# Optimization experiments

Hardware: AMD Instinct MI355X
Metric: run time of the kernel (lower is better)

Reference implementation:

```python
import jax, jax.numpy as jnp
import numpy as np

DIM = 512      # model dim
HEADS = 8
DH = DIM // HEADS          # 64, dim_head
M = DIM // 2               # 256, num_landmarks
ITERS = 6                  # pinv_iterations
K = 33                     # residual_conv_kernel (lucidrains default)
B, N = 4, 4096             # N divisible by M -> no padding branch


def setup_inputs() -> dict:
    key = jax.random.key(0)
    ks = jax.random.split(key, 5)
    s = 0.02
    return {
        "x": jax.random.normal(ks[0], (B, N, DIM), jnp.float32),
        "ln_w": jnp.ones((DIM,), jnp.float32),
        "ln_b": jnp.zeros((DIM,), jnp.float32),
        "w_qkv": jax.random.normal(ks[1], (DIM, 3 * HEADS * DH), jnp.float32) * s,
        "w_out": jax.random.normal(ks[2], (HEADS * DH, DIM), jnp.float32) * s,
        "b_out": jnp.zeros((DIM,), jnp.float32),
        "w_conv": jax.random.normal(ks[3], (HEADS, 1, K, 1), jnp.float32) * s,  # depthwise Conv2d (h,1,33,1)
    }


def _moore_penrose_pinv(x, iters=ITERS):
    # Newton-Schulz iterative pseudo-inverse, as in lucidrains nystrom-attention
    abs_x = jnp.abs(x)
    col = abs_x.sum(-1)
    row = abs_x.sum(-2)
    z = jnp.swapaxes(x, -1, -2) / (jnp.max(col) * jnp.max(row))  # global max, matching torch.max
    I = jnp.eye(x.shape[-1], dtype=x.dtype)
    for _ in range(iters):
        xz = x @ z
        z = 0.25 * z @ (13.0 * I - xz @ (15.0 * I - xz @ (7.0 * I - xz)))
    return z


def reference(x, ln_w, ln_b, w_qkv, w_out, b_out, w_conv):
    b, n, d = x.shape
    # LayerNorm (biased variance, eps=1e-5 as torch default)
    mu = jnp.mean(x, -1, keepdims=True)
    var = jnp.mean(jnp.square(x - mu), -1, keepdims=True)
    xn = (x - mu) / jnp.sqrt(var + 1e-5) * ln_w + ln_b

    qkv = xn @ w_qkv                                   # [b,n,3*h*dh]
    q, k, v = jnp.split(qkv, 3, axis=-1)
    split = lambda t: t.reshape(b, n, HEADS, DH).transpose(0, 2, 1, 3)  # [b,h,n,dh]
    q, k, v = split(q), split(k), split(v)
    q = q * (DH ** -0.5)

    l = n // M                                         # tokens per landmark
    q_l = q.reshape(b, HEADS, M, l, DH).mean(axis=3)   # [b,h,m,dh]
    k_l = k.reshape(b, HEADS, M, l, DH).mean(axis=3)

    sim1 = jnp.einsum('bhid,bhjd->bhij', q, k_l)       # [b,h,n,m]
    sim2 = jnp.einsum('bhid,bhjd->bhij', q_l, k_l)     # [b,h,m,m]
    sim3 = jnp.einsum('bhid,bhjd->bhij', q_l, k)       # [b,h,m,n]
    a1 = jax.nn.softmax(sim1, -1)
    a2 = jax.nn.softmax(sim2, -1)
    a3 = jax.nn.softmax(sim3, -1)

    a2_inv = _moore_penrose_pinv(a2)
    out = (a1 @ a2_inv) @ (a3 @ v)                     # [b,h,n,dh]

    # depthwise residual conv over sequence dim (kernel (33,1), groups=heads)
    res = jax.lax.conv_general_dilated(
        v, w_conv, window_strides=(1, 1),
        padding=((K // 2, K // 2), (0, 0)),
        dimension_numbers=('NCHW', 'OIHW', 'NCHW'),
        feature_group_count=HEADS)
    out = out + res

    out = out.transpose(0, 2, 1, 3).reshape(b, n, HEADS * DH)
    out = out @ w_out + b_out
    return x + out
```

## Files before the change

kernel.cpp:

```cpp
#include <hip/hip_runtime.h>
#include <cstdint>

typedef __bf16 bf16;
typedef __bf16 bf16x8 __attribute__((ext_vector_type(8)));
typedef float  f32x4  __attribute__((ext_vector_type(4)));

__device__ __forceinline__ void glds16(const void* g, void* l) {
  __builtin_amdgcn_global_load_lds((const __attribute__((address_space(1))) void*)g,
                                   (__attribute__((address_space(3))) void*)l, 16, 0, 0);
}

__global__ __launch_bounds__(256) void prep_w(const float* __restrict__ wqkv, const float* __restrict__ wout,
                                              bf16* __restrict__ wqkvT, bf16* __restrict__ woutT) {
  int idx = blockIdx.x * 256 + threadIdx.x;
  if (idx < 98304) {
    int r8 = idx & 63, c = idx >> 6;
    bf16 o[8];
#pragma unroll
    for (int e = 0; e < 8; e++) o[e] = (bf16)wqkv[(long)(r8 * 8 + e) * 1536 + c];
    *(uint4*)(wqkvT + (long)c * 512 + r8 * 8) = *(uint4*)o;
  } else {
    int j = idx - 98304;
    int r8 = j & 63, c = j >> 6;
    bf16 o[8];
#pragma unroll
    for (int e = 0; e < 8; e++) o[e] = (bf16)wout[(long)(r8 * 8 + e) * 512 + c];
    *(uint4*)(woutT + (long)c * 512 + r8 * 8) = *(uint4*)o;
  }
}

__global__ __launch_bounds__(64) void ln_kernel(const float* __restrict__ x,
    const float* __restrict__ w, const float* __restrict__ b, bf16* __restrict__ xn) {
  long row = blockIdx.x;
  int t = threadIdx.x;
  const float* rp = x + row * 512 + t * 8;
  float4 p0 = *(const float4*)rp;
  float4 p1 = *(const float4*)(rp + 4);
  float vals[8] = {p0.x, p0.y, p0.z, p0.w, p1.x, p1.y, p1.z, p1.w};
  float s = 0.f, s2 = 0.f;
#pragma unroll
  for (int e = 0; e < 8; e++) { s += vals[e]; s2 += vals[e] * vals[e]; }
#pragma unroll
  for (int o = 32; o > 0; o >>= 1) { s += __shfl_xor(s, o); s2 += __shfl_xor(s2, o); }
  float mu = s * (1.f / 512.f);
  float var = s2 * (1.f / 512.f) - mu * mu;
  float rstd = rsqrtf(var + 1e-5f);
  float4 w0 = *(const float4*)(w + t * 8), w1 = *(const float4*)(w + t * 8 + 4);
  float4 b0 = *(const float4*)(b + t * 8), b1 = *(const float4*)(b + t * 8 + 4);
  float wv[8] = {w0.x, w0.y, w0.z, w0.w, w1.x, w1.y, w1.z, w1.w};
  float bv[8] = {b0.x, b0.y, b0.z, b0.w, b1.x, b1.y, b1.z, b1.w};
  bf16 outv[8];
#pragma unroll
  for (int e = 0; e < 8; e++) outv[e] = (bf16)((vals[e] - mu) * rstd * wv[e] + bv[e]);
  *(uint4*)(xn + row * 512 + t * 8) = *(uint4*)outv;
}

enum { MODE_BF16 = 1, MODE_QKV = 2, MODE_RESID = 3, MODE_XZ = 4, MODE_DIAG = 5, MODE_Y0 = 6, MODE_ZY = 7 };

template <int KDIM, int MODE>
__global__ __launch_bounds__(256) void gemm_ns(
    const bf16* __restrict__ A, const bf16* __restrict__ B, void* __restrict__ C,
    int N, long sA, long sB, long sC, float alpha, float cdiag,
    const float* __restrict__ scal, bf16* __restrict__ aux0, bf16* __restrict__ aux1) {
  constexpr int BM = 64;
  __shared__ __align__(16) bf16 As[BM * KDIM];
  __shared__ __align__(16) bf16 Bs[BM * KDIM];
  const int tid = threadIdx.x, lane = tid & 63, wave = tid >> 6;
  const int quad = lane >> 4, l16 = lane & 15;
  constexpr int LPR = KDIM / 8;
  constexpr int CPW = (BM * KDIM / 512) / 4;
  constexpr int RPC = 64 / LPR;
  const int bm0 = blockIdx.x * BM, bn0 = blockIdx.y * BM;
  const bf16* Ab = A + (long)blockIdx.z * sA;
  const bf16* Bb = B + (long)(MODE == MODE_ZY ? (blockIdx.z & 31) : blockIdx.z) * sB;

  const int rin = lane / LPR, gr = lane % LPR;
#pragma unroll
  for (int t = 0; t < CPW; t++) {
    int seg = wave * CPW + t;
    int row = seg * RPC + rin;
    int scol = 8 * (gr ^ (row & 7));
    glds16(&Ab[(long)(bm0 + row) * KDIM + scol], &As[seg * 512]);
    glds16(&Bb[(long)(bn0 + row) * KDIM + scol], &Bs[seg * 512]);
  }
  __syncthreads();

  f32x4 zero = {0.f, 0.f, 0.f, 0.f};
  f32x4 acc[4];
#pragma unroll
  for (int j = 0; j < 4; j++) acc[j] = zero;
  const int arow = wave * 16 + l16;
  const int aswz = (l16 & 7) * 8;
#pragma unroll
  for (int ki = 0; ki < KDIM / 32; ki++) {
    int cph = (ki * 32 + quad * 8) ^ aswz;
    bf16x8 af = *(const bf16x8*)&As[arow * KDIM + cph];
    bf16x8 bfr[4];
#pragma unroll
    for (int j = 0; j < 4; j++)
      bfr[j] = *(const bf16x8*)&Bs[(j * 16 + l16) * KDIM + cph];
#pragma unroll
    for (int j = 0; j < 4; j++)
      acc[j] = __builtin_amdgcn_mfma_f32_16x16x32_bf16(af, bfr[j], acc[j], 0, 0, 0);
  }

  const long cb = (long)blockIdx.z * sC;
  float rscale = 1.f;
  if (MODE == MODE_Y0) rscale = 1.f / (scal[0] * scal[1]);
#pragma unroll
  for (int j = 0; j < 4; j++)
#pragma unroll
    for (int r = 0; r < 4; r++) {
      int row = bm0 + wave * 16 + quad * 4 + r;
      int col = bn0 + j * 16 + l16;
      float v = acc[j][r] * alpha;
      if (MODE == MODE_BF16) {
        ((bf16*)C)[cb + (long)row * N + col] = (bf16)v;
      } else if (MODE == MODE_Y0) {
        long o = cb + (long)row * N + col;
        float vv = v * rscale;
        aux0[o] = (bf16)vv;
        aux1[o] = (bf16)(((row == col) ? cdiag : 0.f) - vv);
      } else if (MODE == MODE_ZY) {
        long o = cb + (long)row * N + col;
        ((bf16*)C)[o] = (bf16)v;
        if (blockIdx.z >= 32) aux1[o - 2097152] = (bf16)(((row == col) ? cdiag : 0.f) - v);
      } else if (MODE == MODE_DIAG) {
        ((bf16*)C)[cb + (long)row * N + col] = (bf16)(((row == col) ? cdiag : 0.f) - v);
      }
    }
}

template <int BM, int MODE>
__global__ __launch_bounds__(256) void gemm_g(
    const bf16* __restrict__ A, const bf16* __restrict__ B, void* __restrict__ C,
    int N, int K, long sA, long sB, long sC, float alpha, float cdiag,
    const float* __restrict__ resid, const float* __restrict__ bias,
    bf16* __restrict__ aux0, bf16* __restrict__ aux1, bf16* __restrict__ aux2) {
  constexpr int BK = 32, BN = BM;
  __shared__ __align__(16) bf16 As[BM * BK];
  __shared__ __align__(16) bf16 Bs[BN * BK];
  const int tid = threadIdx.x, lane = tid & 63, wave = tid >> 6;
  const int quad = lane >> 4, l16 = lane & 15;
  constexpr int WN = (BN >= 128) ? 2 : 1;
  constexpr int WM = 4 / WN;
  constexpr int TM = BM / (WM * 16), TN = BN / (WN * 16);
  constexpr int ISS = BM / 64;
  const int wm0 = (wave / WN) * (BM / WM);
  const int wn0 = (wave % WN) * (BN / WN);
  const int bm0 = blockIdx.x * BM, bn0 = blockIdx.y * BN;
  const bf16* Ab = A + (long)blockIdx.z * sA;
  const bf16* Bb = B + (long)blockIdx.z * sB;
  const int srow = lane >> 2, scol = (lane & 3) * 8;

  f32x4 zero = {0.f, 0.f, 0.f, 0.f};
  f32x4 acc[TM][TN];
#pragma unroll
  for (int i = 0; i < TM; i++)
#pragma unroll
    for (int j = 0; j < TN; j++) acc[i][j] = zero;

  for (int k0 = 0; k0 < K; k0 += BK) {
#pragma unroll
    for (int t = 0; t < ISS; t++) {
      int seg = wave * ISS + t;
      glds16(&Ab[(long)(bm0 + seg * 16 + srow) * K + k0 + scol], &As[seg * 512]);
      glds16(&Bb[(long)(bn0 + seg * 16 + srow) * K + k0 + scol], &Bs[seg * 512]);
    }
    __syncthreads();
    bf16x8 af[TM], bfr[TN];
#pragma unroll
    for (int i = 0; i < TM; i++)
      af[i] = *(const bf16x8*)&As[(wm0 + i * 16 + l16) * BK + quad * 8];
#pragma unroll
    for (int j = 0; j < TN; j++)
      bfr[j] = *(const bf16x8*)&Bs[(wn0 + j * 16 + l16) * BK + quad * 8];
#pragma unroll
    for (int i = 0; i < TM; i++)
#pragma unroll
      for (int j = 0; j < TN; j++)
        acc[i][j] = __builtin_amdgcn_mfma_f32_16x16x32_bf16(af[i], bfr[j], acc[i][j], 0, 0, 0);
    __syncthreads();
  }

  const long cb = (long)blockIdx.z * sC;
#pragma unroll
  for (int i = 0; i < TM; i++)
#pragma unroll
    for (int j = 0; j < TN; j++)
#pragma unroll
      for (int r = 0; r < 4; r++) {
        int row = bm0 + wm0 + i * 16 + quad * 4 + r;
        int col = bn0 + wn0 + j * 16 + l16;
        float v = acc[i][j][r] * alpha;
        if (MODE == MODE_QKV) {
          int b = row >> 12, n = row & 4095;
          int which = col >> 9, h = (col >> 6) & 7, d = col & 63;
          long o = ((long)(b * 8 + h) * 4096 + n) * 64 + d;
          if (which == 0) aux0[o] = (bf16)(v * 0.125f);
          else if (which == 1) aux1[o] = (bf16)v;
          else aux2[o] = (bf16)v;
        } else {
          long o = (long)row * N + col;
          ((float*)C)[o] = v + bias[col] + resid[o];
        }
      }
}

template <int BM, int BN, bool BT, int MODE>
__global__ __launch_bounds__(256) void gemm_k(
    const bf16* __restrict__ A, const bf16* __restrict__ B, void* __restrict__ C,
    int M, int N, int K, long sA, long sB, long sC, float alpha, float cdiag,
    const float* __restrict__ resid, const float* __restrict__ bias,
    bf16* __restrict__ aux0, bf16* __restrict__ aux1, bf16* __restrict__ aux2) {
  constexpr int BK = 32, LDST = 40;
  __shared__ __align__(16) bf16 As[BM * LDST];
  __shared__ __align__(16) bf16 Bs[BN * LDST];
  const int tid = threadIdx.x, lane = tid & 63, wave = tid >> 6;
  const int quad = lane >> 4, l16 = lane & 15;
  constexpr int WN = (BN >= 128) ? 2 : 1;
  constexpr int WM = 4 / WN;
  constexpr int TM = BM / (WM * 16), TN = BN / (WN * 16);
  const int wm0 = (wave / WN) * (BM / WM);
  const int wn0 = (wave % WN) * (BN / WN);
  const int bm0 = blockIdx.x * BM, bn0 = blockIdx.y * BN;
  const bf16* Ab = A + (long)blockIdx.z * sA;
  const bf16* Bb = B + (long)blockIdx.z * sB;

  f32x4 zero = {0.f, 0.f, 0.f, 0.f};
  f32x4 acc[TM][TN];
#pragma unroll
  for (int i = 0; i < TM; i++)
#pragma unroll
    for (int j = 0; j < TN; j++) acc[i][j] = zero;

  for (int k0 = 0; k0 < K; k0 += BK) {
    for (int c = tid; c < BM * 4; c += 256) {
      int r = c >> 2, cv = (c & 3) * 8;
      *(uint4*)&As[r * LDST + cv] = *(const uint4*)&Ab[(long)(bm0 + r) * K + k0 + cv];
    }
    if (BT) {
      for (int c = tid; c < BN * 4; c += 256) {
        int r = c >> 2, cv = (c & 3) * 8;
        *(uint4*)&Bs[r * LDST + cv] = *(const uint4*)&Bb[(long)(bn0 + r) * K + k0 + cv];
      }
    } else {
      for (int c = tid; c < BN * 4; c += 256) {
        int kk = c / (BN / 8), nv = (c % (BN / 8)) * 8;
        uint4 tmp = *(const uint4*)&Bb[(long)(k0 + kk) * N + bn0 + nv];
        const bf16* tv = (const bf16*)&tmp;
#pragma unroll
        for (int e = 0; e < 8; e++) Bs[(nv + e) * LDST + kk] = tv[e];
      }
    }
    __syncthreads();
    bf16x8 af[TM], bfr[TN];
#pragma unroll
    for (int i = 0; i < TM; i++)
      af[i] = *(const bf16x8*)&As[(wm0 + i * 16 + l16) * LDST + quad * 8];
#pragma unroll
    for (int j = 0; j < TN; j++)
      bfr[j] = *(const bf16x8*)&Bs[(wn0 + j * 16 + l16) * LDST + quad * 8];
#pragma unroll
    for (int i = 0; i < TM; i++)
#pragma unroll
      for (int j = 0; j < TN; j++)
        acc[i][j] = __builtin_amdgcn_mfma_f32_16x16x32_bf16(af[i], bfr[j], acc[i][j], 0, 0, 0);
    __syncthreads();
  }

  const long cb = (long)blockIdx.z * sC;
#pragma unroll
  for (int i = 0; i < TM; i++)
#pragma unroll
    for (int j = 0; j < TN; j++)
#pragma unroll
      for (int r = 0; r < 4; r++) {
        int row = bm0 + wm0 + i * 16 + quad * 4 + r;
        int col = bn0 + wn0 + j * 16 + l16;
        float v = acc[i][j][r] * alpha;
        if (MODE == MODE_BF16) {
          ((bf16*)C)[cb + (long)row * N + col] = (bf16)v;
        }
      }
}

__global__ __launch_bounds__(256) void lm_kernel(const bf16* __restrict__ q, const bf16* __restrict__ k,
                                                 bf16* __restrict__ ql, bf16* __restrict__ kl) {
  int bh = blockIdx.x, mi = blockIdx.y * 4 + (threadIdx.x >> 6), d = threadIdx.x & 63;
  long base = ((long)bh * 4096 + mi * 16) * 64 + d;
  float sq = 0.f, sk = 0.f;
#pragma unroll
  for (int j = 0; j < 16; j++) { sq += (float)q[base + j * 64]; sk += (float)k[base + j * 64]; }
  long o = ((long)bh * 256 + mi) * 64 + d;
  ql[o] = (bf16)(sq * (1.f / 16.f));
  kl[o] = (bf16)(sk * (1.f / 16.f));
}

__global__ __launch_bounds__(256) void softmax256(bf16* __restrict__ buf) {
  long row = blockIdx.x;
  int t = threadIdx.x, lane = t & 63, wave = t >> 6;
  __shared__ float sm[4];
  float v = (float)buf[row * 256 + t];
  float m = v;
#pragma unroll
  for (int o = 32; o > 0; o >>= 1) m = fmaxf(m, __shfl_xor(m, o));
  if (lane == 0) sm[wave] = m;
  __syncthreads();
  m = fmaxf(fmaxf(sm[0], sm[1]), fmaxf(sm[2], sm[3]));
  float e = __expf(v - m);
  __syncthreads();
  float s = e;
#pragma unroll
  for (int o = 32; o > 0; o >>= 1) s += __shfl_xor(s, o);
  if (lane == 0) sm[wave] = s;
  __syncthreads();
  s = sm[0] + sm[1] + sm[2] + sm[3];
  buf[row * 256 + t] = (bf16)(e / s);
}

__global__ void init_scal(float* scal) { scal[0] = 1.0f; ((int*)scal)[1] = 0; }

__global__ __launch_bounds__(64) void red_col(const bf16* __restrict__ a2h, float* scal) {
  int bh = blockIdx.x;
  int j = blockIdx.y * 64 + threadIdx.x;
  float s = 0.f;
  const bf16* p = a2h + (long)bh * 65536 + j;
  for (int i = 0; i < 256; i++) s += (float)p[i * 256];
  atomicMax((int*)scal + 1, __float_as_int(s));
}

__global__ __launch_bounds__(256) void z0_k(const bf16* __restrict__ a2h,
                                            const float* __restrict__ scal, bf16* __restrict__ z) {
  int bh = blockIdx.x, i = blockIdx.y, j = threadIdx.x;
  float inv = 1.f / (scal[0] * scal[1]);
  float v = (float)a2h[((long)bh * 256 + i) * 256 + j];
  z[((long)bh * 256 + j) * 256 + i] = (bf16)(v * inv);
}

__global__ __launch_bounds__(256) void wt_k(const bf16* __restrict__ W, bf16* __restrict__ WT) {
  int bh = blockIdx.x, tid = threadIdx.x;
  const bf16* wb = W + (long)bh * 16384;
  bf16* wtb = WT + (long)bh * 16384;
  for (int i = tid; i < 2048; i += 256) {
    int n = i >> 3, d8 = (i & 7) * 8;
    uint4 pk = *(const uint4*)&wb[n * 64 + d8];
    const bf16* pv = (const bf16*)&pk;
#pragma unroll
    for (int e = 0; e < 8; e++) wtb[(d8 + e) * 256 + n] = pv[e];
  }
}

__global__ __launch_bounds__(256) void f3_partial(const bf16* __restrict__ ql,
    const bf16* __restrict__ k, const bf16* __restrict__ v,
    float* __restrict__ Opart, float* __restrict__ lpart) {
  const int mt = blockIdx.x, ns = blockIdx.y, bh = blockIdx.z;
  const int tid = threadIdx.x, lane = tid & 63, wave = tid >> 6;
  const int quad = lane >> 4, l16 = lane & 15;
  const int wr0 = mt * 128 + wave * 32;
  __shared__ __align__(16) bf16 vT[64][72];
  __shared__ __align__(16) bf16 Pts[4][32][72];

  const bf16* qlb = ql + (long)bh * 16384;
  const bf16* kb  = k + (long)bh * 262144;
  const bf16* vb  = v + (long)bh * 262144;

  bf16x8 aq[2][2];
#pragma unroll
  for (int ti = 0; ti < 2; ti++)
#pragma unroll
    for (int ki = 0; ki < 2; ki++)
      aq[ti][ki] = *(const bf16x8*)&qlb[(wr0 + ti * 16 + l16) * 64 + ki * 32 + quad * 8];

  f32x4 zero = {0.f, 0.f, 0.f, 0.f};
  f32x4 Oacc[2][4];
#pragma unroll
  for (int i = 0; i < 2; i++)
#pragma unroll
    for (int j = 0; j < 4; j++) Oacc[i][j] = zero;
  float lacc[2][4] = {};

  for (int c = 0; c < 8; c++) {
    int n0c = ns * 512 + c * 64;
    __syncthreads();
    for (int i = tid; i < 512; i += 256) {
      int nn = i >> 3, d8 = (i & 7) * 8;
      uint4 pk = *(const uint4*)&vb[(long)(n0c + nn) * 64 + d8];
      const bf16* pv = (const bf16*)&pk;
#pragma unroll
      for (int e = 0; e < 8; e++) vT[d8 + e][nn] = pv[e];
    }
    __syncthreads();

    f32x4 sacc[2][4];
#pragma unroll
    for (int i = 0; i < 2; i++)
#pragma unroll
      for (int j = 0; j < 4; j++) sacc[i][j] = zero;
#pragma unroll
    for (int ki = 0; ki < 2; ki++) {
      bf16x8 bk[4];
#pragma unroll
      for (int tj = 0; tj < 4; tj++)
        bk[tj] = *(const bf16x8*)&kb[(long)(n0c + tj * 16 + l16) * 64 + ki * 32 + quad * 8];
#pragma unroll
      for (int ti = 0; ti < 2; ti++)
#pragma unroll
        for (int tj = 0; tj < 4; tj++)
          sacc[ti][tj] = __builtin_amdgcn_mfma_f32_16x16x32_bf16(aq[ti][ki], bk[tj], sacc[ti][tj], 0, 0, 0);
    }
#pragma unroll
    for (int ti = 0; ti < 2; ti++)
#pragma unroll
      for (int tj = 0; tj < 4; tj++)
#pragma unroll
        for (int r = 0; r < 4; r++) {
          float e = __expf(sacc[ti][tj][r]);
          lacc[ti][r] += e;
          Pts[wave][ti * 16 + quad * 4 + r][tj * 16 + l16] = (bf16)e;
        }
#pragma unroll
    for (int ki = 0; ki < 2; ki++) {
      bf16x8 ap[2], bv[4];
#pragma unroll
      for (int ti = 0; ti < 2; ti++)
        ap[ti] = *(const bf16x8*)&Pts[wave][ti * 16 + l16][ki * 32 + quad * 8];
#pragma unroll
      for (int tj = 0; tj < 4; tj++)
        bv[tj] = *(const bf16x8*)&vT[tj * 16 + l16][ki * 32 + quad * 8];
#pragma unroll
      for (int ti = 0; ti < 2; ti++)
#pragma unroll
        for (int tj = 0; tj < 4; tj++)
          Oacc[ti][tj] = __builtin_amdgcn_mfma_f32_16x16x32_bf16(ap[ti], bv[tj], Oacc[ti][tj], 0, 0, 0);
    }
  }

#pragma unroll
  for (int ti = 0; ti < 2; ti++)
#pragma unroll
    for (int r = 0; r < 4; r++) {
#pragma unroll
      for (int o = 1; o < 16; o <<= 1) lacc[ti][r] += __shfl_xor(lacc[ti][r], o);
    }
  long pb = ((long)bh * 8 + ns) * 256;
#pragma unroll
  for (int ti = 0; ti < 2; ti++)
#pragma unroll
    for (int r = 0; r < 4; r++) {
      int row = wr0 + ti * 16 + quad * 4 + r;
      if (l16 == 0) lpart[pb + row] = lacc[ti][r];
#pragma unroll
      for (int tj = 0; tj < 4; tj++)
        Opart[(pb + row) * 64 + tj * 16 + l16] = Oacc[ti][tj][r];
    }
}

__global__ __launch_bounds__(256) void f3_combine(const float* __restrict__ Opart,
    const float* __restrict__ lpart, bf16* __restrict__ a3v) {
  int row = blockIdx.x * 4 + (threadIdx.x >> 6);
  int d = threadIdx.x & 63;
  int bh = row >> 8, m = row & 255;
  float so = 0.f, sl = 0.f;
#pragma unroll
  for (int s = 0; s < 8; s++) {
    long pb = ((long)bh * 8 + s) * 256 + m;
    so += Opart[pb * 64 + d];
    sl += lpart[pb];
  }
  a3v[(long)row * 64 + d] = (bf16)(so / sl);
}

__global__ __launch_bounds__(256) void f1_attn(const bf16* __restrict__ q,
    const bf16* __restrict__ kl, const bf16* __restrict__ WT, const bf16* __restrict__ v,
    const float* __restrict__ wconv, bf16* __restrict__ xattn) {
  const int nt = blockIdx.x, bh = blockIdx.y;
  const int h = bh & 7, b = bh >> 3, n0 = nt * 64;
  const int tid = threadIdx.x, lane = tid & 63, wave = tid >> 6;
  const int quad = lane >> 4, l16 = lane & 15;
  __shared__ __align__(16) bf16 PtsBuf[64 * 264];
  __shared__ float red[4][64];
  __shared__ float linv[64];
  bf16 (*Pts)[264] = (bf16(*)[264])PtsBuf;
  bf16 (*vsT)[104] = (bf16(*)[104])PtsBuf;

  const bf16* qb  = q + (long)bh * 262144;
  const bf16* klb = kl + (long)bh * 16384;
  const bf16* wtb = WT + (long)bh * 16384;
  const bf16* vb  = v + (long)bh * 262144;

  float wreg = (lane < 33) ? wconv[h * 33 + lane] : 0.f;

  uint4 vstage[3];
#pragma unroll
  for (int t = 0; t < 3; t++) {
    int i = tid + t * 256;
    int r = i >> 3, d8 = (i & 7) * 8;
    int n = n0 - 16 + r;
    uint4 val = {0u, 0u, 0u, 0u};
    if (n >= 0 && n < 4096) val = *(const uint4*)&vb[(long)n * 64 + d8];
    vstage[t] = val;
  }

  f32x4 zero = {0.f, 0.f, 0.f, 0.f};
  f32x4 sacc[4][4];
#pragma unroll
  for (int i = 0; i < 4; i++)
#pragma unroll
    for (int j = 0; j < 4; j++) sacc[i][j] = zero;
#pragma unroll
  for (int ki = 0; ki < 2; ki++) {
    bf16x8 aq[4], bk[4];
#pragma unroll
    for (int ti = 0; ti < 4; ti++)
      aq[ti] = *(const bf16x8*)&qb[(long)(n0 + ti * 16 + l16) * 64 + ki * 32 + quad * 8];
#pragma unroll
    for (int tj = 0; tj < 4; tj++)
      bk[tj] = *(const bf16x8*)&klb[(long)(wave * 64 + tj * 16 + l16) * 64 + ki * 32 + quad * 8];
#pragma unroll
    for (int ti = 0; ti < 4; ti++)
#pragma unroll
      for (int tj = 0; tj < 4; tj++)
        sacc[ti][tj] = __builtin_amdgcn_mfma_f32_16x16x32_bf16(aq[ti], bk[tj], sacc[ti][tj], 0, 0, 0);
  }
  float ps[4][4] = {};
#pragma unroll
  for (int ti = 0; ti < 4; ti++)
#pragma unroll
    for (int tj = 0; tj < 4; tj++)
#pragma unroll
      for (int r = 0; r < 4; r++) {
        float e = __expf(sacc[ti][tj][r]);
        ps[ti][r] += e;
        Pts[ti * 16 + quad * 4 + r][wave * 64 + tj * 16 + l16] = (bf16)e;
      }
#pragma unroll
  for (int ti = 0; ti < 4; ti++)
#pragma unroll
    for (int r = 0; r < 4; r++) {
#pragma unroll
      for (int o = 1; o < 16; o <<= 1) ps[ti][r] += __shfl_xor(ps[ti][r], o);
      if (l16 == 0) red[wave][ti * 16 + quad * 4 + r] = ps[ti][r];
    }
  __syncthreads();
  if (tid < 64) linv[tid] = 1.f / (red[0][tid] + red[1][tid] + red[2][tid] + red[3][tid]);
  __syncthreads();

  const int r0 = wave * 16;
  f32x4 Oacc[4];
#pragma unroll
  for (int j = 0; j < 4; j++) Oacc[j] = zero;
#pragma unroll
  for (int ki = 0; ki < 8; ki++) {
    bf16x8 ap = *(const bf16x8*)&Pts[r0 + l16][ki * 32 + quad * 8];
    bf16x8 bw[4];
#pragma unroll
    for (int tj = 0; tj < 4; tj++)
      bw[tj] = *(const bf16x8*)&wtb[(long)(tj * 16 + l16) * 256 + ki * 32 + quad * 8];
#pragma unroll
    for (int tj = 0; tj < 4; tj++)
      Oacc[tj] = __builtin_amdgcn_mfma_f32_16x16x32_bf16(ap, bw[tj], Oacc[tj], 0, 0, 0);
  }
  __syncthreads();

#pragma unroll
  for (int t = 0; t < 3; t++) {
    int i = tid + t * 256;
    int r = i >> 3, d8 = (i & 7) * 8;
    const bf16* pv = (const bf16*)&vstage[t];
#pragma unroll
    for (int e = 0; e < 8; e++) vsT[d8 + e][r] = pv[e];
  }
  __syncthreads();

  f32x4 Cacc[4];
#pragma unroll
  for (int j = 0; j < 4; j++) Cacc[j] = zero;
#pragma unroll
  for (int ki = 0; ki < 3; ki++) {
    if (ki * 32 + 31 < r0 || ki * 32 > r0 + 47) continue;
    bf16x8 av;
#pragma unroll
    for (int j = 0; j < 8; j++) {
      int idx = ki * 32 + quad * 8 + j - r0 - l16;
      float wv = __shfl(wreg, idx & 63);
      av[j] = (idx >= 0 && idx < 33) ? (bf16)wv : (bf16)0.f;
    }
    bf16x8 bv[4];
#pragma unroll
    for (int tj = 0; tj < 4; tj++)
      bv[tj] = *(const bf16x8*)&vsT[tj * 16 + l16][ki * 32 + quad * 8];
#pragma unroll
    for (int tj = 0; tj < 4; tj++)
      Cacc[tj] = __builtin_amdgcn_mfma_f32_16x16x32_bf16(av, bv[tj], Cacc[tj], 0, 0, 0);
  }

#pragma unroll
  for (int rr = 0; rr < 4; rr++) {
    int row = r0 + quad * 4 + rr;
    float inv = linv[row];
    int n = n0 + row;
#pragma unroll
    for (int tj = 0; tj < 4; tj++) {
      int d = tj * 16 + l16;
      xattn[(((long)b * 4096 + n) << 9) + (h << 6) + d] = (bf16)(Oacc[tj][rr] * inv + Cacc[tj][rr]);
    }
  }
}

extern "C" void kernel_launch(void* const* d_in, const int* in_sizes, int n_in,
                              void* d_out, int out_size, void* d_ws, size_t ws_size,
                              hipStream_t stream) {
  (void)in_sizes; (void)n_in; (void)out_size; (void)ws_size;
  const float* x      = (const float*)d_in[0];
  const float* ln_w   = (const float*)d_in[1];
  const float* ln_b   = (const float*)d_in[2];
  const float* w_qkv  = (const float*)d_in[3];
  const float* w_out  = (const float*)d_in[4];
  const float* b_out  = (const float*)d_in[5];
  const float* w_conv = (const float*)d_in[6];
  float* out = (float*)d_out;

  char* ws = (char*)d_ws;
  const size_t MB = 1u << 20;
  bf16* q      = (bf16*)(ws + 0 * MB);
  bf16* k      = (bf16*)(ws + 16 * MB);
  bf16* v      = (bf16*)(ws + 32 * MB);
  bf16* xn     = (bf16*)(ws + 48 * MB);
  bf16* a2_h   = (bf16*)(ws + 48 * MB);
  bf16* pbuf   = (bf16*)(ws + 52 * MB);
  bf16* qbuf   = (bf16*)(ws + 56 * MB);
  bf16* rbuf   = (bf16*)(ws + 60 * MB);
  bf16* bufA   = (bf16*)(ws + 64 * MB);
  bf16* bufB   = (bf16*)(ws + 72 * MB);
  float* Opart = (float*)(ws + 48 * MB);
  float* lpart = (float*)(ws + 72 * MB);
  bf16* xattn  = (bf16*)(ws + 73 * MB);
  bf16* wqkvT  = (bf16*)(ws + 73 * MB);
  bf16* ql     = (bf16*)(ws + 89 * MB);
  bf16* kl     = (bf16*)(ws + 90 * MB);
  bf16* a3v    = (bf16*)(ws + 91 * MB);
  bf16* W      = (bf16*)(ws + 92 * MB);
  bf16* WT     = (bf16*)(ws + 93 * MB);
  bf16* woutT  = (bf16*)(ws + 94 * MB);
  float* scal  = (float*)(ws + 94 * MB + 512 * 1024);

  prep_w<<<512, 256, 0, stream>>>(w_qkv, w_out, wqkvT, woutT);
  ln_kernel<<<16384, 64, 0, stream>>>(x, ln_w, ln_b, xn);

  gemm_g<128, MODE_QKV><<<dim3(128, 12, 1), 256, 0, stream>>>(
      xn, wqkvT, nullptr, 1536, 512, 0, 0, 0, 1.f, 0.f, nullptr, nullptr, q, k, v);

  lm_kernel<<<dim3(32, 64), 256, 0, stream>>>(q, k, ql, kl);

  gemm_ns<64, MODE_BF16><<<dim3(4, 4, 32), 256, 0, stream>>>(
      ql, kl, a2_h, 256, 16384, 16384, 65536, 1.f, 0.f, nullptr, nullptr, nullptr);
  softmax256<<<8192, 256, 0, stream>>>(a2_h);

  init_scal<<<1, 1, 0, stream>>>(scal);
  red_col<<<dim3(32, 4), 64, 0, stream>>>(a2_h, scal);
  z0_k<<<dim3(32, 256), 256, 0, stream>>>(a2_h, scal, bufA);
  gemm_ns<256, MODE_Y0><<<dim3(4, 4, 32), 256, 0, stream>>>(
      a2_h, a2_h, nullptr, 256, 65536, 65536, 65536, 1.f, 7.f, scal,
      bufA + 2097152, pbuf);

  bf16* cur = bufA;
  bf16* nxt = bufB;
  for (int it = 0; it < 6; it++) {
    gemm_ns<256, MODE_DIAG><<<dim3(4, 4, 32), 256, 0, stream>>>(
        cur + 2097152, pbuf, qbuf, 256, 65536, 65536, 65536, 1.f, 15.f,
        nullptr, nullptr, nullptr);
    gemm_ns<256, MODE_DIAG><<<dim3(4, 4, 32), 256, 0, stream>>>(
        cur + 2097152, qbuf, rbuf, 256, 65536, 65536, 65536, 1.f, 13.f,
        nullptr, nullptr, nullptr);
    if (it < 5) {
      gemm_ns<256, MODE_ZY><<<dim3(4, 4, 64), 256, 0, stream>>>(
          cur, rbuf, nxt, 256, 65536, 65536, 65536, 0.25f, 7.f,
          nullptr, nullptr, pbuf);
    } else {
      gemm_ns<256, MODE_BF16><<<dim3(4, 4, 32), 256, 0, stream>>>(
          cur, rbuf, nxt, 256, 65536, 65536, 65536, 0.25f, 0.f,
          nullptr, nullptr, nullptr);
    }
    bf16* tmp = cur; cur = nxt; nxt = tmp;
  }

  f3_partial<<<dim3(2, 8, 32), 256, 0, stream>>>(ql, k, v, Opart, lpart);
  f3_combine<<<2048, 256, 0, stream>>>(Opart, lpart, a3v);

  gemm_k<64, 64, false, MODE_BF16><<<dim3(4, 1, 32), 256, 0, stream>>>(
      cur, a3v, W, 256, 64, 256, 65536, 16384, 16384, 1.f, 0.f, nullptr, nullptr, nullptr, nullptr, nullptr);
  wt_k<<<32, 256, 0, stream>>>(W, WT);

  f1_attn<<<dim3(64, 32), 256, 0, stream>>>(q, kl, WT, v, w_conv, xattn);

  gemm_g<128, MODE_RESID><<<dim3(128, 4, 1), 256, 0, stream>>>(
      xattn, woutT, out, 512, 512, 0, 0, 0, 1.f, 0.f, x, b_out, nullptr, nullptr, nullptr);
}
```

Before: 459.3 us.

## Fuse W transpose into GEMM epilogue, tile z0 transpose, split f1 LDS buffers

The W GEMM now writes its output transposed directly through a new epilogue mode, which removes the separate wt_k transpose kernel and its launch. The z0 initial-pinv transpose switches from one block per row with scattered scalar stores to 64x64 LDS-tiled transposes with vectorized loads and stores. f1_attn gets separate LDS arrays for Pts and vsT, so v can be written into shared memory up front instead of being held in registers and stored after a barrier. This raises LDS use per block, which can lower occupancy, and the transposed epilogue uses strided scalar stores.

Result: faster. 439.6 us (-4.3%).

```diff
diff --git a/kernel.cpp b/kernel.cpp
--- a/kernel.cpp
+++ b/kernel.cpp
@@ -55,7 +55,7 @@
   *(uint4*)(xn + row * 512 + t * 8) = *(uint4*)outv;
 }
 
-enum { MODE_BF16 = 1, MODE_QKV = 2, MODE_RESID = 3, MODE_XZ = 4, MODE_DIAG = 5, MODE_Y0 = 6, MODE_ZY = 7 };
+enum { MODE_BF16 = 1, MODE_QKV = 2, MODE_RESID = 3, MODE_XZ = 4, MODE_DIAG = 5, MODE_Y0 = 6, MODE_ZY = 7, MODE_BF16T = 8 };
 
 template <int KDIM, int MODE>
 __global__ __launch_bounds__(256) void gemm_ns(
@@ -281,6 +281,8 @@
         float v = acc[i][j][r] * alpha;
         if (MODE == MODE_BF16) {
           ((bf16*)C)[cb + (long)row * N + col] = (bf16)v;
+        } else if (MODE == MODE_BF16T) {
+          ((bf16*)C)[cb + (long)col * M + row] = (bf16)v;
         }
       }
 }
@@ -332,22 +334,33 @@
 
 __global__ __launch_bounds__(256) void z0_k(const bf16* __restrict__ a2h,
                                             const float* __restrict__ scal, bf16* __restrict__ z) {
-  int bh = blockIdx.x, i = blockIdx.y, j = threadIdx.x;
+  int bh = blockIdx.x, ti = blockIdx.y;
+  int r0 = (ti >> 2) * 64, c0 = (ti & 3) * 64;
+  __shared__ __align__(16) bf16 tile[64][72];
   float inv = 1.f / (scal[0] * scal[1]);
-  float v = (float)a2h[((long)bh * 256 + i) * 256 + j];
-  z[((long)bh * 256 + j) * 256 + i] = (bf16)(v * inv);
-}
-
-__global__ __launch_bounds__(256) void wt_k(const bf16* __restrict__ W, bf16* __restrict__ WT) {
-  int bh = blockIdx.x, tid = threadIdx.x;
-  const bf16* wb = W + (long)bh * 16384;
-  bf16* wtb = WT + (long)bh * 16384;
-  for (int i = tid; i < 2048; i += 256) {
-    int n = i >> 3, d8 = (i & 7) * 8;
-    uint4 pk = *(const uint4*)&wb[n * 64 + d8];
-    const bf16* pv = (const bf16*)&pk;
-#pragma unroll
-    for (int e = 0; e < 8; e++) wtb[(d8 + e) * 256 + n] = pv[e];
+  int tid = threadIdx.x;
+  const bf16* src = a2h + (long)bh * 65536;
+  bf16* dst = z + (long)bh * 65536;
+#pragma unroll
+  for (int t = 0; t < 2; t++) {
+    int i = tid + t * 256;
+    int r = i >> 3, c8 = (i & 7) * 8;
+    uint4 pk = *(const uint4*)&src[(long)(r0 + r) * 256 + c0 + c8];
+    bf16 tmp[8]; *(uint4*)tmp = pk;
+    bf16 sc[8];
+#pragma unroll
+    for (int e = 0; e < 8; e++) sc[e] = (bf16)((float)tmp[e] * inv);
+    *(uint4*)&tile[r][c8] = *(uint4*)sc;
+  }
+  __syncthreads();
+#pragma unroll
+  for (int t = 0; t < 2; t++) {
+    int i = tid + t * 256;
+    int jl = i >> 3, c8 = (i & 7) * 8;
+    bf16 o[8];
+#pragma unroll
+    for (int e = 0; e < 8; e++) o[e] = tile[c8 + e][jl];
+    *(uint4*)&dst[(long)(c0 + jl) * 256 + r0 + c8] = *(uint4*)o;
   }
 }
 
@@ -478,11 +491,10 @@
   const int h = bh & 7, b = bh >> 3, n0 = nt * 64;
   const int tid = threadIdx.x, lane = tid & 63, wave = tid >> 6;
   const int quad = lane >> 4, l16 = lane & 15;
-  __shared__ __align__(16) bf16 PtsBuf[64 * 264];
+  __shared__ __align__(16) bf16 Pts[64][264];
+  __shared__ __align__(16) bf16 vsT[64][104];
   __shared__ float red[4][64];
   __shared__ float linv[64];
-  bf16 (*Pts)[264] = (bf16(*)[264])PtsBuf;
-  bf16 (*vsT)[104] = (bf16(*)[104])PtsBuf;
 
   const bf16* qb  = q + (long)bh * 262144;
   const bf16* klb = kl + (long)bh * 16384;
@@ -491,15 +503,14 @@
 
   float wreg = (lane < 33) ? wconv[h * 33 + lane] : 0.f;
 
-  uint4 vstage[3];
-#pragma unroll
-  for (int t = 0; t < 3; t++) {
-    int i = tid + t * 256;
+  for (int i = tid; i < 768; i += 256) {
     int r = i >> 3, d8 = (i & 7) * 8;
     int n = n0 - 16 + r;
     uint4 val = {0u, 0u, 0u, 0u};
     if (n >= 0 && n < 4096) val = *(const uint4*)&vb[(long)n * 64 + d8];
-    vstage[t] = val;
+    const bf16* pv = (const bf16*)&val;
+#pragma unroll
+    for (int e = 0; e < 8; e++) vsT[d8 + e][r] = pv[e];
   }
 
   f32x4 zero = {0.f, 0.f, 0.f, 0.f};
@@ -561,17 +572,6 @@
     for (int tj = 0; tj < 4; tj++)
       Oacc[tj] = __builtin_amdgcn_mfma_f32_16x16x32_bf16(ap, bw[tj], Oacc[tj], 0, 0, 0);
   }
-  __syncthreads();
-
-#pragma unroll
-  for (int t = 0; t < 3; t++) {
-    int i = tid + t * 256;
-    int r = i >> 3, d8 = (i & 7) * 8;
-    const bf16* pv = (const bf16*)&vstage[t];
-#pragma unroll
-    for (int e = 0; e < 8; e++) vsT[d8 + e][r] = pv[e];
-  }
-  __syncthreads();
 
   f32x4 Cacc[4];
 #pragma unroll
@@ -644,6 +644,7 @@
   bf16* WT     = (bf16*)(ws + 93 * MB);
   bf16* woutT  = (bf16*)(ws + 94 * MB);
   float* scal  = (float*)(ws + 94 * MB + 512 * 1024);
+  (void)W;
 
   prep_w<<<512, 256, 0, stream>>>(w_qkv, w_out, wqkvT, woutT);
   ln_kernel<<<16384, 64, 0, stream>>>(x, ln_w, ln_b, xn);
@@ -659,7 +660,7 @@
 
   init_scal<<<1, 1, 0, stream>>>(scal);
   red_col<<<dim3(32, 4), 64, 0, stream>>>(a2_h, scal);
-  z0_k<<<dim3(32, 256), 256, 0, stream>>>(a2_h, scal, bufA);
+  z0_k<<<dim3(32, 16), 256, 0, stream>>>(a2_h, scal, bufA);
   gemm_ns<256, MODE_Y0><<<dim3(4, 4, 32), 256, 0, stream>>>(
       a2_h, a2_h, nullptr, 256, 65536, 65536, 65536, 1.f, 7.f, scal,
       bufA + 2097152, pbuf);
@@ -688,9 +689,8 @@
   f3_partial<<<dim3(2, 8, 32), 256, 0, stream>>>(ql, k, v, Opart, lpart);
   f3_combine<<<2048, 256, 0, stream>>>(Opart, lpart, a3v);
 
-  gemm_k<64, 64, false, MODE_BF16><<<dim3(4, 1, 32), 256, 0, stream>>>(
-      cur, a3v, W, 256, 64, 256, 65536, 16384, 16384, 1.f, 0.f, nullptr, nullptr, nullptr, nullptr, nullptr);
-  wt_k<<<32, 256, 0, stream>>>(W, WT);
+  gemm_k<64, 64, false, MODE_BF16T><<<dim3(4, 1, 32), 256, 0, stream>>>(
+      cur, a3v, WT, 256, 64, 256, 65536, 16384, 16384, 1.f, 0.f, nullptr, nullptr, nullptr, nullptr, nullptr);
 
   f1_attn<<<dim3(64, 32), 256, 0, stream>>>(q, kl, WT, v, w_conv, xattn);
 
```
